# Kernel optimization log

Measured on AMD Instinct MI355X. Metric: run time of the kernel, lower is better.

Reference implementation:

```python
import jax, jax.numpy as jnp
import numpy as np

MIN_NORM = 1e-15
EPS = 1e-7          # fp32 eps used by hgcn Hyperboloid
MAX_NORM = 1e6
C = 1.0             # curvature for all layers (args.c = 1)
N, D = 16384, 64

# ---- Hyperboloid manifold ops (faithful to hgcn manifolds/hyperboloid.py) ----

def _norm(v):
    return jnp.sqrt(jnp.sum(v * v, axis=-1, keepdims=True))

def proj(x, c):
    K = 1.0 / c
    y = x[..., 1:]
    x0 = jnp.sqrt(jnp.clip(K + jnp.sum(y * y, -1, keepdims=True), EPS))
    return jnp.concatenate([x0, y], -1)

def proj_tan0(u, c):
    return jnp.concatenate([jnp.zeros_like(u[..., :1]), u[..., 1:]], -1)

def expmap0(u, c):
    sqrtK = (1.0 / c) ** 0.5
    x = u[..., 1:]
    xn = jnp.clip(_norm(x), MIN_NORM)
    theta = xn / sqrtK
    res = jnp.concatenate([sqrtK * jnp.cosh(theta),
                           sqrtK * jnp.sinh(theta) * x / xn], -1)
    return proj(res, c)

def logmap0(x, c):
    sqrtK = (1.0 / c) ** 0.5
    y = x[..., 1:]
    yn = jnp.clip(_norm(y), MIN_NORM)
    theta = jnp.clip(x[..., :1] / sqrtK, 1.0 + EPS)
    return jnp.concatenate([jnp.zeros_like(theta),
                            sqrtK * jnp.arccosh(theta) * y / yn], -1)

def mink_dot(x, y):
    return -x[..., :1] * y[..., :1] + jnp.sum(x[..., 1:] * y[..., 1:], -1, keepdims=True)

def expmap(u, x, c):
    sqrtK = (1.0 / c) ** 0.5
    normu = jnp.minimum(jnp.sqrt(jnp.clip(mink_dot(u, u), EPS)), MAX_NORM)
    theta = jnp.clip(normu / sqrtK, MIN_NORM)
    return proj(jnp.cosh(theta) * x + jnp.sinh(theta) * u / theta, c)

def proj_tan(u, x, c):
    ux = jnp.sum(x[..., 1:] * u[..., 1:], -1, keepdims=True)
    return jnp.concatenate([ux / jnp.clip(x[..., :1], EPS), u[..., 1:]], -1)

def ptransp0(x, u, c):
    sqrtK = (1.0 / c) ** 0.5
    x0, y = x[..., :1], x[..., 1:]
    yn = jnp.clip(_norm(y), MIN_NORM)
    yhat = y / yn
    v = jnp.concatenate([-yn, (sqrtK - x0) * yhat], -1)
    alpha = jnp.sum(yhat * u[..., 1:], -1, keepdims=True) / sqrtK
    return proj_tan(u - alpha * v, x, c)

def mobius_add(x, y, c):
    u = logmap0(y, c)
    v = ptransp0(x, u, c)
    return expmap(v, x, c)

# ---- HGCN layers (HypLinear -> HypAgg -> HypAct), dropout=0, use_att=False ----

def hyp_linear(x, W, b, c):
    mv = expmap0(logmap0(x, c) @ W.T, c)   # mobius_matvec
    res = proj(mv, c)
    hyp_bias = proj(expmap0(proj_tan0(b[None, :], c), c), c)
    return proj(mobius_add(res, hyp_bias, c), c)

def hyp_agg(x, adj_n, c):
    return proj(expmap0(adj_n @ logmap0(x, c), c), c)

def hyp_act(x, c_in, c_out):
    xt = proj_tan0(jax.nn.relu(logmap0(x, c_in)), c_out)
    return proj(expmap0(xt, c_out), c_out)

def hgc_layer(x, adj_n, W, b, c_in, c_out):
    h = hyp_linear(x, W, b, c_in)
    h = hyp_agg(h, adj_n, c_in)
    return hyp_act(h, c_in, c_out)

def setup_inputs() -> dict:
    key = jax.random.key(0)
    k1, k2, k3, k4, k5, k6 = jax.random.split(key, 6)
    return {
        "x": jax.random.normal(k1, (N, D), jnp.float32),
        "adj": jax.random.uniform(k2, (N, N), jnp.float32),
        "W1": jax.random.normal(k3, (D, D), jnp.float32) * 0.125,
        "b1": jax.random.normal(k4, (D,), jnp.float32) * 0.01,
        "W2": jax.random.normal(k5, (D, D), jnp.float32) * 0.125,
        "b2": jax.random.normal(k6, (D,), jnp.float32) * 0.01,
    }

def reference(x, adj, W1, b1, W2, b2):
    # project input to hyperboloid
    x_hyp = proj(expmap0(proj_tan0(x, C), C), C)
    # row-normalize adjacency: D^{-1} A (inf -> 0)
    rsum = jnp.sum(adj, axis=1)
    rinv = jnp.where(rsum != 0, 1.0 / rsum, 0.0)
    adj_n = rinv[:, None] * adj
    h1 = hgc_layer(x_hyp, adj_n, W1, b1, C, C)
    h2 = hgc_layer(h1, adj_n, W2, b2, C, C)
    return (h1, h2)
```

## Files before the change

kernel.cpp:

```cpp
#include <hip/hip_runtime.h>
#include <cstdint>
#include <cstddef>

#define NROWS 16384
#define KDIM  16384
#define EPSF  1e-7f
#define MINN  1e-15f
#define MAXN  1e6f
#define KSPLIT 8
#define BK    32
#define KRANGE (KDIM/KSPLIT)
#define NSTEP  (KRANGE/BK)
#define PGS    1040

typedef __attribute__((ext_vector_type(8))) short short8;
typedef __attribute__((ext_vector_type(4))) float f32x4;
typedef __attribute__((ext_vector_type(4))) unsigned short u16x4;

__device__ __forceinline__ unsigned short f2bf(float f){
  union { float f; unsigned u; } c; c.f = f;
  unsigned u = c.u;
  unsigned r = (u + 0x7FFFu + ((u >> 16) & 1u)) >> 16;
  return (unsigned short)r;
}

__device__ __forceinline__ float wredsum(float v){
  v += __shfl_xor(v, 1);
  v += __shfl_xor(v, 2);
  v += __shfl_xor(v, 4);
  v += __shfl_xor(v, 8);
  v += __shfl_xor(v, 16);
  v += __shfl_xor(v, 32);
  return v;
}

__global__ __launch_bounds__(128) void k_bias(const float* __restrict__ b1,
                                              const float* __restrict__ b2,
                                              float* __restrict__ ub){
  int w = threadIdx.x >> 6, l = threadIdx.x & 63;
  const float* b = w ? b2 : b1;
  float bv = b[l];
  float tb = l ? bv : 0.f;
  float s  = wredsum(tb*tb);
  float xn = fmaxf(sqrtf(s), MINN);
  float sc = sinhf(xn)/xn;
  float e  = sc*tb;
  float s2 = wredsum(e*e);
  float x0 = sqrtf(fmaxf(1.f+s2, EPSF));
  float yn = fmaxf(sqrtf(s2), MINN);
  float th = fmaxf(x0, 1.f+EPSF);
  float u  = l ? acoshf(th)*e/yn : 0.f;
  ub[w*64 + l] = u;
}

template<int MODE>
__global__ __launch_bounds__(256) void k_linear(const float* __restrict__ in,
                                                const float* __restrict__ W,
                                                const float* __restrict__ ub,
                                                float* __restrict__ g){
  __shared__ float Wt[64*65];
  int tid = threadIdx.x;
  for(int idx = tid; idx < 4096; idx += 256){
    int j = idx >> 6, k = idx & 63;
    Wt[k*65 + j] = W[idx];
  }
  __syncthreads();
  int lane = tid & 63;
  int row  = blockIdx.x*4 + (tid >> 6);
  float v = in[(size_t)row*64 + lane];
  float lx;
  if (MODE == 0){
    float t  = lane ? v : 0.f;
    float s  = wredsum(t*t);
    float tn = fmaxf(sqrtf(s), MINN);
    float sc = sinhf(tn)/tn;
    float e  = sc*t;
    float s2 = wredsum(e*e);
    float x0 = sqrtf(fmaxf(1.f+s2, EPSF));
    float yn = fmaxf(sqrtf(s2), MINN);
    float th = fmaxf(x0, 1.f+EPSF);
    lx = lane ? acoshf(th)*e/yn : 0.f;
  } else {
    float t  = lane ? v : 0.f;
    float s2 = wredsum(t*t);
    float x0 = __shfl(v, 0);
    float yn = fmaxf(sqrtf(s2), MINN);
    float th = fmaxf(x0, 1.f+EPSF);
    lx = lane ? acoshf(th)*t/yn : 0.f;
  }
  float mv = 0.f;
  #pragma unroll
  for(int k = 0; k < 64; k++){
    mv = fmaf(__shfl(lx, k), Wt[k*65 + lane], mv);
  }
  float u  = lane ? mv : 0.f;
  float s  = wredsum(u*u);
  float un = fmaxf(sqrtf(s), MINN);
  float sc = sinhf(un)/un;
  float e  = sc*u;
  float s2 = wredsum(e*e);
  float r0 = sqrtf(fmaxf(1.f+s2, EPSF));
  float ubt   = lane ? ub[lane] : 0.f;
  float yn    = fmaxf(sqrtf(s2), MINN);
  float yhat  = e/yn;
  float alpha = wredsum(yhat*ubt);
  float w     = ubt - alpha*(1.f - r0)*yhat;
  float ux    = wredsum(e*w);
  float v0    = ux / fmaxf(r0, EPSF);
  float md    = wredsum(w*w) - v0*v0;
  float normu = fminf(sqrtf(fmaxf(md, EPSF)), MAXN);
  float th2   = fmaxf(normu, MINN);
  float ch    = coshf(th2);
  float shq   = sinhf(th2)/th2;
  float ov    = ch*(lane ? e : r0) + shq*(lane ? w : v0);
  float ot    = lane ? ov : 0.f;
  float s3    = wredsum(ot*ot);
  float o0    = sqrtf(fmaxf(1.f+s3, EPSF));
  float yn2 = fmaxf(sqrtf(s3), MINN);
  float th3 = fmaxf(o0, 1.f+EPSF);
  float gv  = lane ? acoshf(th3)*ot/yn2 : 0.f;
  g[(size_t)row*64 + lane] = gv;
}

template<bool FIRST>
__global__ __launch_bounds__(256) void k_matmul(const float* __restrict__ adj,
                                                const float* __restrict__ g,
                                                float* __restrict__ pagg,
                                                float* __restrict__ prsum){
  __shared__ __align__(16) char As[4*PGS];
  __shared__ __align__(16) char Bs[4*PGS];
  int tid  = threadIdx.x;
  int rb   = blockIdx.x;
  int ks   = blockIdx.y;
  int row0 = rb*64;
  size_t k0 = (size_t)ks * KRANGE;
  int lane = tid & 63, w = tid >> 6;

  int r0 = tid >> 3;
  int kq = tid & 7;
  const float* arow0 = adj + (size_t)(row0 + r0)*KDIM + k0 + kq*4;
  const float* arow1 = arow0 + (size_t)32*KDIM;
  char* Awr = As + (kq >> 1)*PGS + r0*16 + (kq & 1)*8;

  int nB  = tid & 63;
  int kgB = tid >> 6;
  const float* gcol = g + (k0 + (size_t)kgB*8)*64 + nB;
  char* Bwr = Bs + kgB*PGS + nB*16;

  const char* Ard  = As + (lane >> 4)*PGS + (w*16 + (lane & 15))*16;
  const char* Brd0 = Bs + (lane >> 4)*PGS + (lane & 15)*16;

  f32x4 acc[4];
  #pragma unroll
  for(int i = 0; i < 4; i++) acc[i] = (f32x4){0.f,0.f,0.f,0.f};
  float rsA = 0.f, rsB = 0.f;

  float4 a0 = *(const float4*)(arow0);
  float4 a1 = *(const float4*)(arow1);
  float gb[8];
  #pragma unroll
  for(int j = 0; j < 8; j++) gb[j] = gcol[j*64];

  for(int ch = 0; ch < NSTEP; ch++){
    if (FIRST){
      rsA += a0.x + a0.y + a0.z + a0.w;
      rsB += a1.x + a1.y + a1.z + a1.w;
    }
    __syncthreads();
    u16x4 ap0 = { f2bf(a0.x), f2bf(a0.y), f2bf(a0.z), f2bf(a0.w) };
    u16x4 ap1 = { f2bf(a1.x), f2bf(a1.y), f2bf(a1.z), f2bf(a1.w) };
    *(u16x4*)(Awr)       = ap0;
    *(u16x4*)(Awr + 512) = ap1;
    short8 bp;
    #pragma unroll
    for(int j = 0; j < 8; j++) bp[j] = (short)f2bf(gb[j]);
    *(short8*)(Bwr) = bp;
    __syncthreads();
    short8 af  = *(const short8*)(Ard);
    short8 bf0 = *(const short8*)(Brd0);
    short8 bf1 = *(const short8*)(Brd0 + 256);
    short8 bf2 = *(const short8*)(Brd0 + 512);
    short8 bf3 = *(const short8*)(Brd0 + 768);
    if (ch + 1 < NSTEP){
      a0 = *(const float4*)(arow0 + (size_t)(ch+1)*BK);
      a1 = *(const float4*)(arow1 + (size_t)(ch+1)*BK);
      #pragma unroll
      for(int j = 0; j < 8; j++) gb[j] = gcol[(size_t)(ch+1)*BK*64 + j*64];
    }
    acc[0] = __builtin_amdgcn_mfma_f32_16x16x32_bf16(af, bf0, acc[0], 0, 0, 0);
    acc[1] = __builtin_amdgcn_mfma_f32_16x16x32_bf16(af, bf1, acc[1], 0, 0, 0);
    acc[2] = __builtin_amdgcn_mfma_f32_16x16x32_bf16(af, bf2, acc[2], 0, 0, 0);
    acc[3] = __builtin_amdgcn_mfma_f32_16x16x32_bf16(af, bf3, acc[3], 0, 0, 0);
  }

  if (FIRST){
    rsA += __shfl_xor(rsA, 1); rsA += __shfl_xor(rsA, 2); rsA += __shfl_xor(rsA, 4);
    rsB += __shfl_xor(rsB, 1); rsB += __shfl_xor(rsB, 2); rsB += __shfl_xor(rsB, 4);
    if (kq == 0){
      prsum[(size_t)ks*NROWS + row0 + r0]      = rsA;
      prsum[(size_t)ks*NROWS + row0 + r0 + 32] = rsB;
    }
  }
  float* ob = pagg + ((size_t)ks*NROWS + row0 + w*16)*64;
  #pragma unroll
  for(int nb = 0; nb < 4; nb++){
    int n = nb*16 + (lane & 15);
    #pragma unroll
    for(int r = 0; r < 4; r++){
      int m = (lane >> 4)*4 + r;
      ob[(size_t)m*64 + n] = acc[nb][r];
    }
  }
}

__global__ __launch_bounds__(256) void k_rinv(const float* __restrict__ prsum,
                                              float* __restrict__ rinv){
  int i = blockIdx.x*256 + threadIdx.x;
  float s = 0.f;
  #pragma unroll
  for(int ks = 0; ks < KSPLIT; ks++) s += prsum[(size_t)ks*NROWS + i];
  rinv[i] = (s != 0.f) ? 1.f/s : 0.f;
}

__global__ __launch_bounds__(256) void k_finalize(const float* __restrict__ pagg,
                                                  const float* __restrict__ rinv,
                                                  float* __restrict__ agg){
  size_t e = (size_t)blockIdx.x*256 + threadIdx.x;
  int i = (int)(e >> 6);
  float s = 0.f;
  #pragma unroll
  for(int ks = 0; ks < KSPLIT; ks++) s += pagg[(size_t)ks*NROWS*64 + e];
  agg[e] = s * rinv[i];
}

__global__ __launch_bounds__(256) void k_postagg(const float* __restrict__ agg,
                                                 float* __restrict__ h){
  int tid = threadIdx.x; int lane = tid & 63;
  int row = blockIdx.x*4 + (tid >> 6);
  float a  = agg[(size_t)row*64 + lane];
  float at = lane ? a : 0.f;
  float s  = wredsum(at*at);
  float un = fmaxf(sqrtf(s), MINN);
  float sc = sinhf(un)/un;
  float e  = sc*at;
  float s2 = wredsum(e*e);
  float x0 = sqrtf(fmaxf(1.f+s2, EPSF));
  float yn = fmaxf(sqrtf(s2), MINN);
  float th = fmaxf(x0, 1.f+EPSF);
  float lt = lane ? acoshf(th)*e/yn : 0.f;
  float r  = fmaxf(lt, 0.f);
  float s3 = wredsum(r*r);
  float rn = fmaxf(sqrtf(s3), MINN);
  float sc2= sinhf(rn)/rn;
  float e2 = sc2*r;
  float s4 = wredsum(e2*e2);
  float h0 = sqrtf(fmaxf(1.f+s4, EPSF));
  h[(size_t)row*64 + lane] = lane ? e2 : h0;
}

extern "C" void kernel_launch(void* const* d_in, const int* in_sizes, int n_in,
                              void* d_out, int out_size, void* d_ws, size_t ws_size,
                              hipStream_t stream){
  const float* x   = (const float*)d_in[0];
  const float* adj = (const float*)d_in[1];
  const float* W1  = (const float*)d_in[2];
  const float* b1  = (const float*)d_in[3];
  const float* W2  = (const float*)d_in[4];
  const float* b2  = (const float*)d_in[5];
  float* out = (float*)d_out;
  float* h1  = out;
  float* h2  = out + (size_t)NROWS*64;

  float* wsf   = (float*)d_ws;
  float* gbuf  = wsf;
  float* pagg  = gbuf  + (size_t)NROWS*64;
  float* prsum = pagg  + (size_t)KSPLIT*NROWS*64;
  float* rinv  = prsum + (size_t)KSPLIT*NROWS;
  float* ubs   = rinv  + NROWS;

  dim3 gm(NROWS/64, KSPLIT);

  k_bias<<<1, 128, 0, stream>>>(b1, b2, ubs);
  k_linear<0><<<NROWS/4, 256, 0, stream>>>(x, W1, ubs, gbuf);
  k_matmul<true><<<gm, 256, 0, stream>>>(adj, gbuf, pagg, prsum);
  k_rinv<<<NROWS/256, 256, 0, stream>>>(prsum, rinv);
  k_finalize<<<NROWS*64/256, 256, 0, stream>>>(pagg, rinv, gbuf);
  k_postagg<<<NROWS/4, 256, 0, stream>>>(gbuf, h1);
  k_linear<1><<<NROWS/4, 256, 0, stream>>>(h1, W2, ubs + 64, gbuf);
  k_matmul<false><<<gm, 256, 0, stream>>>(adj, gbuf, pagg, prsum);
  k_finalize<<<NROWS*64/256, 256, 0, stream>>>(pagg, rinv, gbuf);
  k_postagg<<<NROWS/4, 256, 0, stream>>>(gbuf, h2);
}
```

Measured before the change: 603.3 us.

## Pre-transpose g to bf16 and feed MFMA operands directly from global memory

Adds a transpose kernel that writes g as k-contiguous bf16, so the adjacency matmul can load A and B fragments straight from global memory into registers. This removes the LDS staging and both block barriers per K step. It also fuses the row-sum inverse, split-K reduction and post-aggregation into one kernel, cutting launches and one intermediate write. In exchange there is an extra transpose pass. Each wave now reads adj rows as 32-byte strided segments and keeps four B fragments live per step, which may hurt coalescing and raise register pressure.

Result: slower. 889.1 us (+47.4%).

```diff
diff --git a/kernel.cpp b/kernel.cpp
--- a/kernel.cpp
+++ b/kernel.cpp
@@ -11,17 +11,15 @@
 #define BK    32
 #define KRANGE (KDIM/KSPLIT)
 #define NSTEP  (KRANGE/BK)
-#define PGS    1040
 
 typedef __attribute__((ext_vector_type(8))) short short8;
 typedef __attribute__((ext_vector_type(4))) float f32x4;
-typedef __attribute__((ext_vector_type(4))) unsigned short u16x4;
-
-__device__ __forceinline__ unsigned short f2bf(float f){
+
+__device__ __forceinline__ short f2bf(float f){
   union { float f; unsigned u; } c; c.f = f;
   unsigned u = c.u;
   unsigned r = (u + 0x7FFFu + ((u >> 16) & 1u)) >> 16;
-  return (unsigned short)r;
+  return (short)r;
 }
 
 __device__ __forceinline__ float wredsum(float v){
@@ -122,83 +120,93 @@
   g[(size_t)row*64 + lane] = gv;
 }
 
+__global__ __launch_bounds__(256) void k_tr(const float* __restrict__ g,
+                                            short* __restrict__ gT){
+  __shared__ float t[64][65];
+  int tid = threadIdx.x;
+  int b   = blockIdx.x;
+  int r   = tid >> 2;
+  int c0  = (tid & 3)*16;
+  const float* src = g + ((size_t)b*64 + r)*64 + c0;
+  #pragma unroll
+  for(int i = 0; i < 4; i++){
+    float4 v = *(const float4*)(src + i*4);
+    t[r][c0 + i*4 + 0] = v.x; t[r][c0 + i*4 + 1] = v.y;
+    t[r][c0 + i*4 + 2] = v.z; t[r][c0 + i*4 + 3] = v.w;
+  }
+  __syncthreads();
+  int n   = tid >> 2;
+  int seg = tid & 3;
+  short8 p0, p1;
+  #pragma unroll
+  for(int j = 0; j < 8; j++) p0[j] = f2bf(t[seg*16 + j][n]);
+  #pragma unroll
+  for(int j = 0; j < 8; j++) p1[j] = f2bf(t[seg*16 + 8 + j][n]);
+  short* dst = gT + (size_t)n*KDIM + b*64 + seg*16;
+  *(short8*)(dst)     = p0;
+  *(short8*)(dst + 8) = p1;
+}
+
 template<bool FIRST>
 __global__ __launch_bounds__(256) void k_matmul(const float* __restrict__ adj,
-                                                const float* __restrict__ g,
+                                                const short* __restrict__ gT,
                                                 float* __restrict__ pagg,
                                                 float* __restrict__ prsum){
-  __shared__ __align__(16) char As[4*PGS];
-  __shared__ __align__(16) char Bs[4*PGS];
   int tid  = threadIdx.x;
+  int lane = tid & 63, w = tid >> 6;
   int rb   = blockIdx.x;
   int ks   = blockIdx.y;
   int row0 = rb*64;
   size_t k0 = (size_t)ks * KRANGE;
-  int lane = tid & 63, w = tid >> 6;
-
-  int r0 = tid >> 3;
-  int kq = tid & 7;
-  const float* arow0 = adj + (size_t)(row0 + r0)*KDIM + k0 + kq*4;
-  const float* arow1 = arow0 + (size_t)32*KDIM;
-  char* Awr = As + (kq >> 1)*PGS + r0*16 + (kq & 1)*8;
-
-  int nB  = tid & 63;
-  int kgB = tid >> 6;
-  const float* gcol = g + (k0 + (size_t)kgB*8)*64 + nB;
-  char* Bwr = Bs + kgB*PGS + nB*16;
-
-  const char* Ard  = As + (lane >> 4)*PGS + (w*16 + (lane & 15))*16;
-  const char* Brd0 = Bs + (lane >> 4)*PGS + (lane & 15)*16;
+  int r  = lane & 15;
+  int kg = lane >> 4;
+
+  const float* aptr = adj + (size_t)(row0 + w*16 + r)*KDIM + k0 + (size_t)kg*8;
+  const short* bptr = gT + (size_t)r*KDIM + k0 + (size_t)kg*8;
 
   f32x4 acc[4];
   #pragma unroll
   for(int i = 0; i < 4; i++) acc[i] = (f32x4){0.f,0.f,0.f,0.f};
-  float rsA = 0.f, rsB = 0.f;
-
-  float4 a0 = *(const float4*)(arow0);
-  float4 a1 = *(const float4*)(arow1);
-  float gb[8];
-  #pragma unroll
-  for(int j = 0; j < 8; j++) gb[j] = gcol[j*64];
+  float rs = 0.f;
+
+  float4 a0 = *(const float4*)(aptr);
+  float4 a1 = *(const float4*)(aptr + 4);
+  short8 b0 = *(const short8*)(bptr);
+  short8 b1 = *(const short8*)(bptr + (size_t)16*KDIM);
+  short8 b2 = *(const short8*)(bptr + (size_t)32*KDIM);
+  short8 b3 = *(const short8*)(bptr + (size_t)48*KDIM);
 
   for(int ch = 0; ch < NSTEP; ch++){
+    float4 a0n, a1n; short8 b0n, b1n, b2n, b3n;
+    if (ch + 1 < NSTEP){
+      const float* ap = aptr + (size_t)(ch+1)*BK;
+      a0n = *(const float4*)(ap);
+      a1n = *(const float4*)(ap + 4);
+      const short* bp = bptr + (size_t)(ch+1)*BK;
+      b0n = *(const short8*)(bp);
+      b1n = *(const short8*)(bp + (size_t)16*KDIM);
+      b2n = *(const short8*)(bp + (size_t)32*KDIM);
+      b3n = *(const short8*)(bp + (size_t)48*KDIM);
+    }
     if (FIRST){
-      rsA += a0.x + a0.y + a0.z + a0.w;
-      rsB += a1.x + a1.y + a1.z + a1.w;
-    }
-    __syncthreads();
-    u16x4 ap0 = { f2bf(a0.x), f2bf(a0.y), f2bf(a0.z), f2bf(a0.w) };
-    u16x4 ap1 = { f2bf(a1.x), f2bf(a1.y), f2bf(a1.z), f2bf(a1.w) };
-    *(u16x4*)(Awr)       = ap0;
-    *(u16x4*)(Awr + 512) = ap1;
-    short8 bp;
-    #pragma unroll
-    for(int j = 0; j < 8; j++) bp[j] = (short)f2bf(gb[j]);
-    *(short8*)(Bwr) = bp;
-    __syncthreads();
-    short8 af  = *(const short8*)(Ard);
-    short8 bf0 = *(const short8*)(Brd0);
-    short8 bf1 = *(const short8*)(Brd0 + 256);
-    short8 bf2 = *(const short8*)(Brd0 + 512);
-    short8 bf3 = *(const short8*)(Brd0 + 768);
-    if (ch + 1 < NSTEP){
-      a0 = *(const float4*)(arow0 + (size_t)(ch+1)*BK);
-      a1 = *(const float4*)(arow1 + (size_t)(ch+1)*BK);
-      #pragma unroll
-      for(int j = 0; j < 8; j++) gb[j] = gcol[(size_t)(ch+1)*BK*64 + j*64];
-    }
-    acc[0] = __builtin_amdgcn_mfma_f32_16x16x32_bf16(af, bf0, acc[0], 0, 0, 0);
-    acc[1] = __builtin_amdgcn_mfma_f32_16x16x32_bf16(af, bf1, acc[1], 0, 0, 0);
-    acc[2] = __builtin_amdgcn_mfma_f32_16x16x32_bf16(af, bf2, acc[2], 0, 0, 0);
-    acc[3] = __builtin_amdgcn_mfma_f32_16x16x32_bf16(af, bf3, acc[3], 0, 0, 0);
+      rs += a0.x + a0.y + a0.z + a0.w + a1.x + a1.y + a1.z + a1.w;
+    }
+    short8 af;
+    af[0] = f2bf(a0.x); af[1] = f2bf(a0.y); af[2] = f2bf(a0.z); af[3] = f2bf(a0.w);
+    af[4] = f2bf(a1.x); af[5] = f2bf(a1.y); af[6] = f2bf(a1.z); af[7] = f2bf(a1.w);
+    acc[0] = __builtin_amdgcn_mfma_f32_16x16x32_bf16(af, b0, acc[0], 0, 0, 0);
+    acc[1] = __builtin_amdgcn_mfma_f32_16x16x32_bf16(af, b1, acc[1], 0, 0, 0);
+    acc[2] = __builtin_amdgcn_mfma_f32_16x16x32_bf16(af, b2, acc[2], 0, 0, 0);
+    acc[3] = __builtin_amdgcn_mfma_f32_16x16x32_bf16(af, b3, acc[3], 0, 0, 0);
+    a0 = a0n; a1 = a1n;
+    b0 = b0n; b1 = b1n; b2 = b2n; b3 = b3n;
   }
 
   if (FIRST){
-    rsA += __shfl_xor(rsA, 1); rsA += __shfl_xor(rsA, 2); rsA += __shfl_xor(rsA, 4);
-    rsB += __shfl_xor(rsB, 1); rsB += __shfl_xor(rsB, 2); rsB += __shfl_xor(rsB, 4);
-    if (kq == 0){
-      prsum[(size_t)ks*NROWS + row0 + r0]      = rsA;
-      prsum[(size_t)ks*NROWS + row0 + r0 + 32] = rsB;
+    rs += __shfl_xor(rs, 16);
+    rs += __shfl_xor(rs, 32);
+    if (lane < 16){
+      prsum[(size_t)ks*NROWS + row0 + w*16 + lane] = rs;
     }
   }
   float* ob = pagg + ((size_t)ks*NROWS + row0 + w*16)*64;
@@ -206,41 +214,37 @@
   for(int nb = 0; nb < 4; nb++){
     int n = nb*16 + (lane & 15);
     #pragma unroll
-    for(int r = 0; r < 4; r++){
-      int m = (lane >> 4)*4 + r;
-      ob[(size_t)m*64 + n] = acc[nb][r];
-    }
-  }
-}
-
-__global__ __launch_bounds__(256) void k_rinv(const float* __restrict__ prsum,
-                                              float* __restrict__ rinv){
-  int i = blockIdx.x*256 + threadIdx.x;
-  float s = 0.f;
-  #pragma unroll
-  for(int ks = 0; ks < KSPLIT; ks++) s += prsum[(size_t)ks*NROWS + i];
-  rinv[i] = (s != 0.f) ? 1.f/s : 0.f;
-}
-
-__global__ __launch_bounds__(256) void k_finalize(const float* __restrict__ pagg,
-                                                  const float* __restrict__ rinv,
-                                                  float* __restrict__ agg){
-  size_t e = (size_t)blockIdx.x*256 + threadIdx.x;
-  int i = (int)(e >> 6);
-  float s = 0.f;
-  #pragma unroll
-  for(int ks = 0; ks < KSPLIT; ks++) s += pagg[(size_t)ks*NROWS*64 + e];
-  agg[e] = s * rinv[i];
-}
-
-__global__ __launch_bounds__(256) void k_postagg(const float* __restrict__ agg,
-                                                 float* __restrict__ h){
+    for(int q = 0; q < 4; q++){
+      int m = (lane >> 4)*4 + q;
+      ob[(size_t)m*64 + n] = acc[nb][q];
+    }
+  }
+}
+
+template<int LAYER>
+__global__ __launch_bounds__(256) void k_post(const float* __restrict__ pagg,
+                                              const float* __restrict__ prsum,
+                                              float* __restrict__ rinv,
+                                              float* __restrict__ h){
   int tid = threadIdx.x; int lane = tid & 63;
   int row = blockIdx.x*4 + (tid >> 6);
-  float a  = agg[(size_t)row*64 + lane];
+  float s = 0.f;
+  #pragma unroll
+  for(int ks = 0; ks < KSPLIT; ks++) s += pagg[(size_t)ks*NROWS*64 + (size_t)row*64 + lane];
+  float ri;
+  if (LAYER == 1){
+    float rsum = 0.f;
+    #pragma unroll
+    for(int ks = 0; ks < KSPLIT; ks++) rsum += prsum[(size_t)ks*NROWS + row];
+    ri = (rsum != 0.f) ? 1.f/rsum : 0.f;
+    if (lane == 0) rinv[row] = ri;
+  } else {
+    ri = rinv[row];
+  }
+  float a  = s * ri;
   float at = lane ? a : 0.f;
-  float s  = wredsum(at*at);
-  float un = fmaxf(sqrtf(s), MINN);
+  float ss = wredsum(at*at);
+  float un = fmaxf(sqrtf(ss), MINN);
   float sc = sinhf(un)/un;
   float e  = sc*at;
   float s2 = wredsum(e*e);
@@ -248,11 +252,11 @@
   float yn = fmaxf(sqrtf(s2), MINN);
   float th = fmaxf(x0, 1.f+EPSF);
   float lt = lane ? acoshf(th)*e/yn : 0.f;
-  float r  = fmaxf(lt, 0.f);
-  float s3 = wredsum(r*r);
+  float rl = fmaxf(lt, 0.f);
+  float s3 = wredsum(rl*rl);
   float rn = fmaxf(sqrtf(s3), MINN);
   float sc2= sinhf(rn)/rn;
-  float e2 = sc2*r;
+  float e2 = sc2*rl;
   float s4 = wredsum(e2*e2);
   float h0 = sqrtf(fmaxf(1.f+s4, EPSF));
   h[(size_t)row*64 + lane] = lane ? e2 : h0;
@@ -277,17 +281,17 @@
   float* prsum = pagg  + (size_t)KSPLIT*NROWS*64;
   float* rinv  = prsum + (size_t)KSPLIT*NROWS;
   float* ubs   = rinv  + NROWS;
+  short* gT    = (short*)(ubs + 128);
 
   dim3 gm(NROWS/64, KSPLIT);
 
   k_bias<<<1, 128, 0, stream>>>(b1, b2, ubs);
   k_linear<0><<<NROWS/4, 256, 0, stream>>>(x, W1, ubs, gbuf);
-  k_matmul<true><<<gm, 256, 0, stream>>>(adj, gbuf, pagg, prsum);
-  k_rinv<<<NROWS/256, 256, 0, stream>>>(prsum, rinv);
-  k_finalize<<<NROWS*64/256, 256, 0, stream>>>(pagg, rinv, gbuf);
-  k_postagg<<<NROWS/4, 256, 0, stream>>>(gbuf, h1);
+  k_tr<<<NROWS/64, 256, 0, stream>>>(gbuf, gT);
+  k_matmul<true><<<gm, 256, 0, stream>>>(adj, gT, pagg, prsum);
+  k_post<1><<<NROWS/4, 256, 0, stream>>>(pagg, prsum, rinv, h1);
   k_linear<1><<<NROWS/4, 256, 0, stream>>>(h1, W2, ubs + 64, gbuf);
-  k_matmul<false><<<gm, 256, 0, stream>>>(adj, gbuf, pagg, prsum);
-  k_finalize<<<NROWS*64/256, 256, 0, stream>>>(pagg, rinv, gbuf);
-  k_postagg<<<NROWS/4, 256, 0, stream>>>(gbuf, h2);
-}
+  k_tr<<<NROWS/64, 256, 0, stream>>>(gbuf, gT);
+  k_matmul<false><<<gm, 256, 0, stream>>>(adj, gT, pagg, prsum);
+  k_post<2><<<NROWS/4, 256, 0, stream>>>(pagg, prsum, rinv, h2);
+}
```
